# Optimization experiments

Hardware: AMD Instinct MI355X
Metric: run time of the kernel (lower is better)

The kernel has to match this reference:

```python
import jax, jax.numpy as jnp
import numpy as np
import math

NUM_HEADS = 16
SEGMENT_SIZE = 128
DILATION = 2


def hilbert_map(seq_len: int) -> np.ndarray:
    """Boustrophedon ('Hilbert') permutation, matching the torch reference."""
    if seq_len <= 64:
        return np.arange(seq_len, dtype=np.int64)
    g = int(math.ceil(math.sqrt(seq_len)))
    fm = np.zeros(seq_len, dtype=np.int64)
    idx = 0
    for row in range(g):
        cols = range(g) if row % 2 == 0 else range(g - 1, -1, -1)
        for col in cols:
            lp = row * g + col
            if lp < seq_len and idx < seq_len:
                fm[lp] = idx
                idx += 1
    return fm


def setup_inputs() -> dict:
    key = jax.random.key(0)
    k1, k2, k3 = jax.random.split(key, 3)
    B, S, D = 2, 8192, 1024
    x = jax.random.normal(k1, (B, S, D), dtype=jnp.float32)
    W_qkv = jax.random.normal(k2, (D, 3 * D), dtype=jnp.float32) * 0.02
    W_out = jax.random.normal(k3, (D, D), dtype=jnp.float32) * 0.02
    return {"x": x, "W_qkv": W_qkv, "W_out": W_out}


def reference(x, W_qkv, W_out):
    B, S, Dm = x.shape
    H, Dh = NUM_HEADS, Dm // NUM_HEADS
    seg, dil = SEGMENT_SIZE, DILATION
    scale = Dh ** -0.5

    qkv = (x @ W_qkv).reshape(B, S, 3, H, Dh)
    q = jnp.transpose(qkv[:, :, 0], (0, 2, 1, 3))  # [B,H,S,Dh]
    k = jnp.transpose(qkv[:, :, 1], (0, 2, 1, 3))
    v = jnp.transpose(qkv[:, :, 2], (0, 2, 1, 3))

    # Hilbert reorder (active since S > 64)
    m = jnp.asarray(hilbert_map(S))
    q, k, v = q[:, :, m], k[:, :, m], v[:, :, m]

    # Vectorized segment-local dilated attention (S % seg == 0 here)
    nseg = S // seg
    qs = q.reshape(B, H, nseg, seg, Dh)
    ks = k.reshape(B, H, nseg, seg, Dh)[:, :, :, ::dil]  # dilated keys
    vs = v.reshape(B, H, nseg, seg, Dh)[:, :, :, ::dil]
    scores = jnp.einsum('bhnqd,bhnkd->bhnqk', qs, ks) * scale
    attn = jax.nn.softmax(scores, axis=-1)
    out = jnp.einsum('bhnqk,bhnkd->bhnqd', attn, vs).reshape(B, H, S, Dh)

    # Reverse Hilbert ordering
    inv = jnp.argsort(m)
    out = out[:, :, inv]

    out = jnp.transpose(out, (0, 2, 1, 3)).reshape(B, S, Dm)
    return out @ W_out
```

## Files before the change

kernel.cpp:

```cpp
#include <hip/hip_runtime.h>
#include <stdint.h>

typedef unsigned short ushort_t;
typedef __bf16 bf16x8 __attribute__((ext_vector_type(8)));
typedef float  f32x4  __attribute__((ext_vector_type(4)));

#define DEV static __device__ __forceinline__

DEV ushort_t f2bf(float f){
  union { float f; unsigned u; } x; x.f = f;
  unsigned u = x.u;
  return (ushort_t)((u + 0x7fffu + ((u >> 16) & 1u)) >> 16);
}

DEV int hmap(int p){
  int r = p / 91;
  int c = p - r * 91;
  return (r & 1) ? (r * 91 + 90 - c) : p;
}

template<int GATHER>
DEV int arow_map(int r){
  if (GATHER == 0) return r;
  if (GATHER == 1){ int b = r >> 13, p = r & 8191; return b * 8192 + hmap(p); }
  int b = r >> 12, rem = r & 4095, seg = rem >> 6, j = rem & 63;
  return b * 8192 + hmap(seg * 128 + 2 * j);
}

DEV void async16(const void* g, void* l){
  __builtin_amdgcn_global_load_lds(
      (const __attribute__((address_space(1))) unsigned*)g,
      (__attribute__((address_space(3))) unsigned*)l, 16, 0, 0);
}

__global__ void cast_kernel(const float* __restrict__ in, ushort_t* __restrict__ out, int n4){
  int stride = gridDim.x * blockDim.x;
  for (int i = blockIdx.x * blockDim.x + threadIdx.x; i < n4; i += stride){
    float4 v = ((const float4*)in)[i];
    ushort4 o;
    o.x = f2bf(v.x); o.y = f2bf(v.y); o.z = f2bf(v.z); o.w = f2bf(v.w);
    ((ushort4*)out)[i] = o;
  }
}

__global__ void transpose_cast(const float* __restrict__ W, ushort_t* __restrict__ WT,
                               int rows, int cols){
  __shared__ ushort_t t[64 * 66];
  int tid = threadIdx.x;
  int c0 = blockIdx.x * 64, r0 = blockIdx.y * 64;
  int cl = tid & 63, rb = tid >> 6;
  for (int i = 0; i < 16; ++i){
    int r = rb + i * 4;
    t[r * 66 + cl] = f2bf(W[(size_t)(r0 + r) * cols + c0 + cl]);
  }
  __syncthreads();
  int rr = tid & 63, cb = tid >> 6;
  for (int i = 0; i < 16; ++i){
    int cc = cb + i * 4;
    WT[(size_t)(c0 + cc) * rows + r0 + rr] = t[rr * 66 + cc];
  }
}


#define BARRIER() asm volatile("s_barrier" ::: "memory")
#define LGKM0()   asm volatile("s_waitcnt lgkmcnt(0)" ::: "memory")
#define VMCNT0()  asm volatile("s_waitcnt vmcnt(0)" ::: "memory")

#define STAGE_A_TO(DST, T1)                                                    \
  if ((T1) < NT){                                                              \
    _Pragma("unroll") for (int i = 0; i < 4; ++i)                              \
      async16(&A[asrcR[i] + (size_t)(T1) * 64], &DST[i * 4096 + tid * 8]);     \
  }

#define STAGE_B_TO(DST, T1)                                                    \
  if ((T1) < NT){                                                              \
    _Pragma("unroll") for (int i = 0; i < 4; ++i)                              \
      async16(&BT[bsrcR[i] + (size_t)(T1) * 64], &DST[i * 4096 + tid * 8]);    \
  }

#define READ_AF(ABUF, MI0)                                                     \
  _Pragma("unroll") for (int m2 = 0; m2 < 2; ++m2)                             \
    _Pragma("unroll") for (int kk = 0; kk < 2; ++kk)                           \
      af[m2][kk] = *(const bf16x8*)&ABUF[(wm * 128 + ((MI0) + m2) * 16 + md) * 64 + axor[kk]];

#define MFMA16(MI0)                                                            \
  __builtin_amdgcn_s_setprio(1);                                               \
  _Pragma("unroll") for (int kk = 0; kk < 2; ++kk)                             \
    _Pragma("unroll") for (int ni = 0; ni < 4; ++ni)                           \
      _Pragma("unroll") for (int m2 = 0; m2 < 2; ++m2)                         \
        acc[(MI0) + m2][ni] = __builtin_amdgcn_mfma_f32_16x16x32_bf16(         \
            af[m2][kk], bv[ni][kk], acc[(MI0) + m2][ni], 0, 0, 0);             \
  __builtin_amdgcn_s_setprio(0);

#define TILE(T, CUR, NXT)                                                      \
  {                                                                            \
    bf16x8 af[2][2], bv[4][2];                                                 \
    _Pragma("unroll") for (int ni = 0; ni < 4; ++ni)                           \
      _Pragma("unroll") for (int kk = 0; kk < 2; ++kk)                         \
        bv[ni][kk] = *(const bf16x8*)&Bs##CUR[(wn * 64 + ni * 16 + md) * 64 + axor[kk]]; \
    READ_AF(As##CUR, 0);                                                       \
    STAGE_A_TO(As##NXT, (T) + 1);                                              \
    BARRIER(); LGKM0(); MFMA16(0); BARRIER();                                  \
    READ_AF(As##CUR, 2);                                                       \
    STAGE_B_TO(Bs##NXT, (T) + 1);                                              \
    BARRIER(); LGKM0(); MFMA16(2); BARRIER();                                  \
    READ_AF(As##CUR, 4);                                                       \
    BARRIER(); LGKM0(); MFMA16(4); BARRIER();                                  \
    READ_AF(As##CUR, 6);                                                       \
    BARRIER(); LGKM0(); MFMA16(6); VMCNT0(); BARRIER();                        \
  }

template<int OUT_BF16, int GATHER>
__global__ __launch_bounds__(512, 2) void gemm_bt(const ushort_t* __restrict__ A,
                                                  const ushort_t* __restrict__ BT,
                                                  void* __restrict__ Cout,
                                                  int M, int N, int K){
  __shared__ __align__(16) ushort_t As0[16384];
  __shared__ __align__(16) ushort_t As1[16384];
  __shared__ __align__(16) ushort_t Bs0[16384];
  __shared__ __align__(16) ushort_t Bs1[16384];
  const int NT = K >> 6;
  int tid = threadIdx.x;
  int lane = tid & 63, w = tid >> 6;
  int md = lane & 15, qd = lane >> 4;
  int wm = w >> 2, wn = w & 3;

  int o = blockIdx.x;
  int mtc = M >> 8;
  int nt = o / mtc, mt = o - nt * mtc;
  int m0 = mt << 8, n0 = nt << 8;

  int rbase = tid >> 3;
  int g0 = ((tid & 7) ^ (rbase & 7)) * 8;
  size_t asrcR[4], bsrcR[4];
  #pragma unroll
  for (int i = 0; i < 4; ++i){
    asrcR[i] = (size_t)arow_map<GATHER>(m0 + i * 64 + rbase) * K + g0;
    bsrcR[i] = (size_t)(n0 + i * 64 + rbase) * K + g0;
  }

  int axor[2] = { (qd ^ (md & 7)) * 8, ((4 + qd) ^ (md & 7)) * 8 };

  f32x4 acc[8][4];
  #pragma unroll
  for (int a = 0; a < 8; ++a)
    #pragma unroll
    for (int b = 0; b < 4; ++b)
      #pragma unroll
      for (int e = 0; e < 4; ++e) acc[a][b][e] = 0.f;

  STAGE_A_TO(As0, 0);
  STAGE_B_TO(Bs0, 0);
  VMCNT0(); BARRIER();

  for (int t = 0; t < NT; t += 2){
    TILE(t,     0, 1);
    TILE(t + 1, 1, 0);
  }

  int crow0 = m0 + wm * 128 + qd * 4;
  int ccol0 = n0 + wn * 64 + md;
  #pragma unroll
  for (int mi = 0; mi < 8; ++mi){
    #pragma unroll
    for (int ni = 0; ni < 4; ++ni){
      f32x4 v = acc[mi][ni];
      #pragma unroll
      for (int r = 0; r < 4; ++r){
        size_t idx = (size_t)(crow0 + mi * 16 + r) * N + ccol0 + ni * 16;
        if (OUT_BF16) ((ushort_t*)Cout)[idx] = f2bf(v[r]);
        else          ((float*)   Cout)[idx] = v[r];
      }
    }
  }
}

__global__ __launch_bounds__(256) void attn_kernel(const ushort_t* __restrict__ Qb,
                                                   const ushort_t* __restrict__ KV,
                                                   ushort_t* __restrict__ aout){
  __shared__ ushort_t Qs[128 * 72];
  __shared__ ushort_t Ks[64 * 72];
  __shared__ ushort_t Vt[64 * 72];
  int tid  = threadIdx.x;
  int lane = tid & 63, w = tid >> 6;
  int qd = lane >> 4, md = lane & 15;
  int seg = blockIdx.x, h = blockIdx.y, b = blockIdx.z;
  int p0 = seg * 128;

  for (int it = 0; it < 4; ++it){
    int q = it * 256 + tid;
    int r = q >> 3, ch = q & 7;
    uint4 d = *(const uint4*)&Qb[(size_t)(b * 8192 + p0 + r) * 1024 + h * 64 + ch * 8];
    *(uint4*)&Qs[r * 72 + ch * 8] = d;
  }
  for (int it = 0; it < 2; ++it){
    int q = it * 256 + tid;
    int r = q >> 3, ch = q & 7;
    uint4 d = *(const uint4*)&KV[(size_t)(b * 4096 + seg * 64 + r) * 2048 + h * 64 + ch * 8];
    *(uint4*)&Ks[r * 72 + ch * 8] = d;
  }
  for (int it = 0; it < 2; ++it){
    int q = it * 256 + tid;
    int r = q >> 3, ch = q & 7;
    union { uint4 v; ushort_t u[8]; } d;
    d.v = *(const uint4*)&KV[(size_t)(b * 4096 + seg * 64 + r) * 2048 + 1024 + h * 64 + ch * 8];
    int kslot = ((r >> 3) ^ ch) * 8 + (r & 7);
    for (int e = 0; e < 8; ++e) Vt[(ch * 8 + e) * 72 + kslot] = d.u[e];
  }
  __syncthreads();

  f32x4 z = {0.f, 0.f, 0.f, 0.f};
  f32x4 sc[2][4];
  for (int mi = 0; mi < 2; ++mi) for (int ni = 0; ni < 4; ++ni) sc[mi][ni] = z;
  for (int kc = 0; kc < 2; ++kc){
    bf16x8 aq[2], bk[4];
    for (int mi = 0; mi < 2; ++mi)
      aq[mi] = *(const bf16x8*)&Qs[(w * 32 + mi * 16 + md) * 72 + kc * 32 + qd * 8];
    for (int ni = 0; ni < 4; ++ni)
      bk[ni] = *(const bf16x8*)&Ks[(ni * 16 + md) * 72 + kc * 32 + qd * 8];
    for (int mi = 0; mi < 2; ++mi)
      for (int ni = 0; ni < 4; ++ni)
        sc[mi][ni] = __builtin_amdgcn_mfma_f32_16x16x32_bf16(aq[mi], bk[ni], sc[mi][ni], 0, 0, 0);
  }

  const float scale = 0.125f;
  ushort_t* Ps = Qs;
  for (int mi = 0; mi < 2; ++mi){
    for (int i = 0; i < 4; ++i){
      float mx = sc[mi][0][i];
      for (int ni = 1; ni < 4; ++ni) mx = fmaxf(mx, sc[mi][ni][i]);
      for (int d = 1; d < 16; d <<= 1) mx = fmaxf(mx, __shfl_xor(mx, d));
      float e[4], sum = 0.f;
      for (int ni = 0; ni < 4; ++ni){ e[ni] = __expf((sc[mi][ni][i] - mx) * scale); sum += e[ni]; }
      for (int d = 1; d < 16; d <<= 1) sum += __shfl_xor(sum, d);
      float inv = 1.0f / sum;
      int r = w * 32 + mi * 16 + qd * 4 + i;
      for (int ni = 0; ni < 4; ++ni)
        Ps[r * 72 + ni * 16 + md] = f2bf(e[ni] * inv);
    }
  }

  f32x4 oc[2][4];
  for (int mi = 0; mi < 2; ++mi) for (int ni = 0; ni < 4; ++ni) oc[mi][ni] = z;
  for (int kc = 0; kc < 2; ++kc){
    bf16x8 ap[2], bv[4];
    for (int mi = 0; mi < 2; ++mi)
      ap[mi] = *(const bf16x8*)&Ps[(w * 32 + mi * 16 + md) * 72 + kc * 32 + qd * 8];
    for (int ni = 0; ni < 4; ++ni){
      int dd = ni * 16 + md;
      int vchunk = ((kc * 4 + qd) ^ ((dd >> 3) & 7)) & 7;
      bv[ni] = *(const bf16x8*)&Vt[dd * 72 + vchunk * 8];
    }
    for (int mi = 0; mi < 2; ++mi)
      for (int ni = 0; ni < 4; ++ni)
        oc[mi][ni] = __builtin_amdgcn_mfma_f32_16x16x32_bf16(ap[mi], bv[ni], oc[mi][ni], 0, 0, 0);
  }

  for (int mi = 0; mi < 2; ++mi){
    for (int i = 0; i < 4; ++i){
      int rl = w * 32 + mi * 16 + qd * 4 + i;
      for (int ni = 0; ni < 4; ++ni)
        Ps[rl * 72 + ni * 16 + md] = f2bf(oc[mi][ni][i]);
    }
  }
  __syncthreads();
  for (int it = 0; it < 4; ++it){
    int q = it * 256 + tid;
    int r = q >> 3, ch = q & 7;
    int s = hmap(p0 + r);
    *(uint4*)&aout[(size_t)(b * 8192 + s) * 1024 + h * 64 + ch * 8] =
        *(const uint4*)&Qs[r * 72 + ch * 8];
  }
}

extern "C" void kernel_launch(void* const* d_in, const int* in_sizes, int n_in,
                              void* d_out, int out_size, void* d_ws, size_t ws_size,
                              hipStream_t stream){
  const float* x    = (const float*)d_in[0];
  const float* Wqkv = (const float*)d_in[1];
  const float* Wout = (const float*)d_in[2];
  float* out = (float*)d_out;

  char* ws = (char*)d_ws;
  ushort_t* xb    = (ushort_t*)(ws);
  ushort_t* WqT   = (ushort_t*)(ws + 33554432);
  ushort_t* WoT   = (ushort_t*)(ws + 39845888);
  ushort_t* Qbuf  = (ushort_t*)(ws + 41943040);
  ushort_t* KVbuf = (ushort_t*)(ws + 75497472);
  ushort_t* aoutb = (ushort_t*)(ws + 109051904);

  cast_kernel<<<2048, 256, 0, stream>>>(x, xb, (16384 * 1024) / 4);
  transpose_cast<<<dim3(48, 16), 256, 0, stream>>>(Wqkv, WqT, 1024, 3072);
  transpose_cast<<<dim3(16, 16), 256, 0, stream>>>(Wout, WoT, 1024, 1024);
  gemm_bt<1, 1><<<dim3(256), dim3(512), 0, stream>>>(xb, WqT, Qbuf, 16384, 1024, 1024);
  gemm_bt<1, 2><<<dim3(256), dim3(512), 0, stream>>>(xb, WqT + (size_t)1024 * 1024, KVbuf, 8192, 2048, 1024);
  attn_kernel<<<dim3(64, 16, 2), 256, 0, stream>>>(Qbuf, KVbuf, aoutb);
  gemm_bt<0, 0><<<dim3(256), dim3(512), 0, stream>>>(aoutb, WoT, out, 16384, 1024, 1024);
}
```

Before: 264.8 us.

## Restructure GEMM main loop into prefetch-then-compute steps with fewer barriers

Replaces the four-phase tile body, which interleaved A/B staging with quarter-tile MFMA groups, priority bumps and eight barriers, with one step per K-tile. Each step issues the async global-to-LDS loads for the next tile up front, then waits with vmcnt(8) so only the current tile's loads must have landed. It then computes the whole 64-deep tile between two barriers. The aim is to cut barrier and waitcnt overhead and give the loads a full tile of MFMA work to hide behind. In exchange it drops the setprio hints and the finer interleaving of LDS reads with MFMAs, and it depends on the vmcnt count matching the eight outstanding loads.

```diff
diff --git a/kernel.cpp b/kernel.cpp
--- a/kernel.cpp
+++ b/kernel.cpp
@@ -63,51 +63,45 @@
 
 
 #define BARRIER() asm volatile("s_barrier" ::: "memory")
-#define LGKM0()   asm volatile("s_waitcnt lgkmcnt(0)" ::: "memory")
+#define VMCNT8()  asm volatile("s_waitcnt vmcnt(8)" ::: "memory")
 #define VMCNT0()  asm volatile("s_waitcnt vmcnt(0)" ::: "memory")
 
 #define STAGE_A_TO(DST, T1)                                                    \
-  if ((T1) < NT){                                                              \
+  {                                                                            \
     _Pragma("unroll") for (int i = 0; i < 4; ++i)                              \
       async16(&A[asrcR[i] + (size_t)(T1) * 64], &DST[i * 4096 + tid * 8]);     \
   }
 
 #define STAGE_B_TO(DST, T1)                                                    \
-  if ((T1) < NT){                                                              \
+  {                                                                            \
     _Pragma("unroll") for (int i = 0; i < 4; ++i)                              \
       async16(&BT[bsrcR[i] + (size_t)(T1) * 64], &DST[i * 4096 + tid * 8]);    \
   }
 
-#define READ_AF(ABUF, MI0)                                                     \
-  _Pragma("unroll") for (int m2 = 0; m2 < 2; ++m2)                             \
-    _Pragma("unroll") for (int kk = 0; kk < 2; ++kk)                           \
-      af[m2][kk] = *(const bf16x8*)&ABUF[(wm * 128 + ((MI0) + m2) * 16 + md) * 64 + axor[kk]];
-
-#define MFMA16(MI0)                                                            \
-  __builtin_amdgcn_s_setprio(1);                                               \
-  _Pragma("unroll") for (int kk = 0; kk < 2; ++kk)                             \
-    _Pragma("unroll") for (int ni = 0; ni < 4; ++ni)                           \
-      _Pragma("unroll") for (int m2 = 0; m2 < 2; ++m2)                         \
-        acc[(MI0) + m2][ni] = __builtin_amdgcn_mfma_f32_16x16x32_bf16(         \
-            af[m2][kk], bv[ni][kk], acc[(MI0) + m2][ni], 0, 0, 0);             \
-  __builtin_amdgcn_s_setprio(0);
-
-#define TILE(T, CUR, NXT)                                                      \
-  {                                                                            \
-    bf16x8 af[2][2], bv[4][2];                                                 \
+#define COMPUTE(ABUF, BBUF)                                                    \
+  {                                                                            \
+    bf16x8 bv[4][2];                                                           \
     _Pragma("unroll") for (int ni = 0; ni < 4; ++ni)                           \
       _Pragma("unroll") for (int kk = 0; kk < 2; ++kk)                         \
-        bv[ni][kk] = *(const bf16x8*)&Bs##CUR[(wn * 64 + ni * 16 + md) * 64 + axor[kk]]; \
-    READ_AF(As##CUR, 0);                                                       \
-    STAGE_A_TO(As##NXT, (T) + 1);                                              \
-    BARRIER(); LGKM0(); MFMA16(0); BARRIER();                                  \
-    READ_AF(As##CUR, 2);                                                       \
-    STAGE_B_TO(Bs##NXT, (T) + 1);                                              \
-    BARRIER(); LGKM0(); MFMA16(2); BARRIER();                                  \
-    READ_AF(As##CUR, 4);                                                       \
-    BARRIER(); LGKM0(); MFMA16(4); BARRIER();                                  \
-    READ_AF(As##CUR, 6);                                                       \
-    BARRIER(); LGKM0(); MFMA16(6); VMCNT0(); BARRIER();                        \
+        bv[ni][kk] = *(const bf16x8*)&BBUF[(wn * 64 + ni * 16 + md) * 64 + axor[kk]]; \
+    _Pragma("unroll") for (int kk = 0; kk < 2; ++kk)                           \
+      _Pragma("unroll") for (int mi = 0; mi < 8; ++mi){                        \
+        bf16x8 af = *(const bf16x8*)&ABUF[(wm * 128 + mi * 16 + md) * 64 + axor[kk]]; \
+        _Pragma("unroll") for (int ni = 0; ni < 4; ++ni)                       \
+          acc[mi][ni] = __builtin_amdgcn_mfma_f32_16x16x32_bf16(               \
+              af, bv[ni][kk], acc[mi][ni], 0, 0, 0);                           \
+      }                                                                        \
+  }
+
+#define TILE_STEP(CUR, NXT, TSTAGE)                                            \
+  {                                                                            \
+    if ((TSTAGE) < NT){                                                        \
+      STAGE_A_TO(As##NXT, TSTAGE); STAGE_B_TO(Bs##NXT, TSTAGE);                \
+      VMCNT8();                                                                \
+    } else { VMCNT0(); }                                                       \
+    BARRIER();                                                                 \
+    COMPUTE(As##CUR, Bs##CUR);                                                 \
+    BARRIER();                                                                 \
   }
 
 template<int OUT_BF16, int GATHER>
@@ -154,8 +148,8 @@
   VMCNT0(); BARRIER();
 
   for (int t = 0; t < NT; t += 2){
-    TILE(t,     0, 1);
-    TILE(t + 1, 1, 0);
+    TILE_STEP(0, 1, t + 1);
+    TILE_STEP(1, 0, t + 2);
   }
 
   int crow0 = m0 + wm * 128 + qd * 4;
```

New measurement: 266.4 us. No clear change (+0.6%).
